# Performance work log

Measured on AMD Instinct MI355X. Metric: run time of the kernel, lower is better.

## Reference

```python
import jax, jax.numpy as jnp
import numpy as np

H = 128
N = 100000
E = 1000000
IN_DIM = 2 * H + 2


def setup_inputs() -> dict:
    key = jax.random.key(0)
    ks = jax.random.split(key, 10)
    node_embed = jax.random.normal(ks[0], (N, H), dtype=jnp.float32)
    edge_index_score = jax.random.randint(ks[1], (2, E), 0, N, dtype=jnp.int64)
    edge_attr_score = jax.random.uniform(ks[2], (E, 2), dtype=jnp.float32)
    # MLP params (kaiming-ish scale)
    W1 = jax.random.normal(ks[3], (IN_DIM, H), dtype=jnp.float32) / np.sqrt(IN_DIM)
    b1 = jnp.zeros((H,), dtype=jnp.float32)
    ln_gamma = jnp.ones((H,), dtype=jnp.float32)
    ln_beta = jnp.zeros((H,), dtype=jnp.float32)
    W2 = jax.random.normal(ks[4], (H, H // 2), dtype=jnp.float32) / np.sqrt(H)
    b2 = jnp.zeros((H // 2,), dtype=jnp.float32)
    W3 = jax.random.normal(ks[5], (H // 2, 1), dtype=jnp.float32) / np.sqrt(H // 2)
    b3 = jnp.zeros((1,), dtype=jnp.float32)
    return {
        "node_embed": node_embed,
        "edge_index_score": edge_index_score,
        "edge_attr_score": edge_attr_score,
        "W1": W1, "b1": b1, "ln_gamma": ln_gamma, "ln_beta": ln_beta,
        "W2": W2, "b2": b2, "W3": W3, "b3": b3,
    }


def _layernorm(x, gamma, beta, eps=1e-5):
    mu = jnp.mean(x, axis=-1, keepdims=True)
    var = jnp.mean(jnp.square(x - mu), axis=-1, keepdims=True)
    return (x - mu) * jax.lax.rsqrt(var + eps) * gamma + beta


def reference(node_embed, edge_index_score, edge_attr_score,
              W1, b1, ln_gamma, ln_beta, W2, b2, W3, b3):
    i_idx = edge_index_score[0]
    j_idx = edge_index_score[1]
    # [E, 2H+2]
    e_in = jnp.concatenate([node_embed[i_idx], node_embed[j_idx], edge_attr_score], axis=-1)
    h = _layernorm(e_in @ W1 + b1, ln_gamma, ln_beta)
    h = jax.nn.relu(h)  # dropout is identity in eval mode
    h = jax.nn.relu(h @ W2 + b2)
    logit = h @ W3 + b3
    return logit.squeeze(-1)  # [E]
```

## Files before the change

### kernel.cpp

```cpp
#include <hip/hip_runtime.h>
#include <hip/hip_bf16.h>
#include <hip/hip_fp16.h>

typedef __attribute__((ext_vector_type(8))) short short8;
typedef __attribute__((ext_vector_type(4))) float f32x4;
typedef _Float16 h2v __attribute__((ext_vector_type(2)));
typedef _Float16 h8v __attribute__((ext_vector_type(8)));
typedef unsigned short ushort_t;

namespace {

constexpr int H     = 128;
constexpr int E     = 1000000;
constexpr int NNODE = 100000;
constexpr int EB    = 512;
constexpr int NTILE = (E + EB - 1) / EB;
constexpr int GRID  = 256;
constexpr int TPB   = NTILE / GRID;
constexpr int REM   = NTILE - TPB * GRID;

constexpr size_t AT_OFF  = 0;
constexpr size_t AT_SZ   = (size_t)NNODE * 256 * 2;
constexpr size_t W1F_OFF = AT_SZ;
constexpr size_t W1F_SZ  = 64 * 64 * 8 * 2;
constexpr size_t W2F_OFF = W1F_OFF + W1F_SZ;
constexpr size_t W2F_SZ  = 20 * 64 * 8 * 2;
constexpr size_t WS_NEED = W2F_OFF + W2F_SZ;

__device__ __forceinline__ ushort_t f2bf(float x) {
    unsigned u = __float_as_uint(x);
    return (ushort_t)((u + 0x7FFFu + ((u >> 16) & 1u)) >> 16);
}
__device__ __forceinline__ unsigned pkbf(float a, float b) {
    __hip_bfloat162 t = __float22bfloat162_rn(make_float2(a, b));
    return *reinterpret_cast<unsigned*>(&t);
}
__device__ __forceinline__ unsigned pkhf(float a, float b) {
    __half2 t = __float22half2_rn(make_float2(a, b));
    return *reinterpret_cast<unsigned*>(&t);
}
__device__ __forceinline__ int imin(int a, int b) { return a < b ? a : b; }

union FragU { int4 i; short8 s; };
union SlotU { short8 s; h2v h[4]; };
union H8U   { h8v v; h2v h[4]; int4 i; };
union U32H  { unsigned u; h2v h; };

typedef const __attribute__((address_space(1))) unsigned int* gptr_t;
typedef __attribute__((address_space(3))) unsigned int* lptr_t;

__device__ __forceinline__ void gload16(const void* g, void* l) {
    __builtin_amdgcn_global_load_lds((gptr_t)g, (lptr_t)l, 16, 0, 0);
}

__global__ void cvt_wfrag(const float* __restrict__ W1, const float* __restrict__ W2,
                          const float* __restrict__ b2,
                          ushort_t* __restrict__ w1f, ushort_t* __restrict__ w2f) {
    int u = blockIdx.x, l = threadIdx.x;
    int lo = l & 15, hi = l >> 4;
    if (u < 64) {
        int s = u >> 3, n = u & 7, col = n * 16 + lo;
#pragma unroll
        for (int j = 0; j < 8; ++j) {
            int kk = s * 32 + hi * 8 + j;
            w1f[(u * 64 + l) * 8 + j] = f2bf(W1[kk * 128 + col]);
        }
    } else {
        int u2 = u - 64;
        int s = u2 >> 2, n = u2 & 3, col = n * 16 + lo;
#pragma unroll
        for (int j = 0; j < 8; ++j) {
            int kk = s * 32 + hi * 8 + j;
            float v = (kk < 128) ? W2[kk * 64 + col]
                    : (kk == 128 ? b2[col] : 0.f);
            __half hh = __float2half_rn(v);
            w2f[(u2 * 64 + l) * 8 + j] = *reinterpret_cast<ushort_t*>(&hh);
        }
    }
}

struct PrepSm { ushort_t w1f[32768]; };

__global__ __launch_bounds__(512, 2)
void build_atab(const float* __restrict__ ne, const ushort_t* __restrict__ w1fg,
                const float* __restrict__ b1, ushort_t* __restrict__ atab) {
    __shared__ PrepSm sm;
    const int tid = threadIdx.x;
    {
        const uint4* s1 = reinterpret_cast<const uint4*>(w1fg);
        uint4*       d1 = reinterpret_cast<uint4*>(sm.w1f);
#pragma unroll
        for (int i = 0; i < 8; ++i) d1[i * 512 + tid] = s1[i * 512 + tid];
    }
    __syncthreads();

    const int wid = tid >> 6, lane = tid & 63;
    const int lo = lane & 15, hi = lane >> 4;
    const int nbase = blockIdx.x * 512 + wid * 64;
    const f32x4 z4 = {0.f, 0.f, 0.f, 0.f};

    short8 nf[4][4];
#pragma unroll
    for (int mt = 0; mt < 4; ++mt) {
        int node = imin(nbase + mt * 16 + lo, NNODE - 1);
        const float* row = ne + (size_t)node * H;
#pragma unroll
        for (int s = 0; s < 4; ++s) {
            f32x4 a = *reinterpret_cast<const f32x4*>(row + s * 32 + hi * 8);
            f32x4 b = *reinterpret_cast<const f32x4*>(row + s * 32 + hi * 8 + 4);
            FragU f;
            f.i = make_int4((int)pkbf(a[0], a[1]), (int)pkbf(a[2], a[3]),
                            (int)pkbf(b[0], b[1]), (int)pkbf(b[2], b[3]));
            nf[mt][s] = f.s;
        }
    }

#pragma unroll
    for (int X = 0; X < 2; ++X) {
        f32x4 acc[4][8];
        if (X == 0) {
#pragma unroll
            for (int n = 0; n < 8; ++n) {
                f32x4 b1v = *reinterpret_cast<const f32x4*>(b1 + n * 16 + hi * 4);
#pragma unroll
                for (int mt = 0; mt < 4; ++mt) acc[mt][n] = b1v;
            }
        } else {
#pragma unroll
            for (int mt = 0; mt < 4; ++mt)
#pragma unroll
                for (int n = 0; n < 8; ++n) acc[mt][n] = z4;
        }
#pragma unroll
        for (int s = 0; s < 4; ++s)
#pragma unroll
            for (int n = 0; n < 8; ++n) {
                short8 wa = *reinterpret_cast<const short8*>(
                    sm.w1f + (((X * 4 + s) * 8 + n) * 64 + lane) * 8);
#pragma unroll
                for (int mt = 0; mt < 4; ++mt)
                    acc[mt][n] = __builtin_amdgcn_mfma_f32_16x16x32_bf16(wa, nf[mt][s], acc[mt][n], 0, 0, 0);
            }
#pragma unroll
        for (int mt = 0; mt < 4; ++mt) {
            int node = nbase + mt * 16 + lo;
            if (node < NNODE) {
                ushort_t* dst = atab + (size_t)node * 256 + X * 128;
#pragma unroll
                for (int n = 0; n < 8; ++n) {
                    uint2 v = make_uint2(pkhf(acc[mt][n][0], acc[mt][n][1]),
                                         pkhf(acc[mt][n][2], acc[mt][n][3]));
                    *reinterpret_cast<uint2*>(dst + n * 16 + hi * 4) = v;
                }
            }
        }
    }
}

struct __align__(16) SmemT {
    char     gbuf[8][2][8192];
    ushort_t w2f[10240];
    unsigned t0h[64], t1h[64], gh[64], bh[64];
    float    w3s[64];
};

#define GISSUE(slotp, iv, jv)                                                   \
    {                                                                           \
        const ushort_t* gi_ = atab + (size_t)(iv) * 256 + hi * 8;               \
        const ushort_t* gj_ = atab + (size_t)(jv) * 256 + 128 + hi * 8;         \
        char* lb_ = (slotp);                                                    \
        _Pragma("unroll")                                                       \
        for (int s_ = 0; s_ < 4; ++s_) gload16(gi_ + s_ * 32, lb_ + s_ * 1024); \
        _Pragma("unroll")                                                       \
        for (int s_ = 0; s_ < 4; ++s_) gload16(gj_ + s_ * 32, lb_ + 4096 + s_ * 1024); \
    }

#define SUBTILE(MT, slotp, WAITLIT, IV, JV)                                     \
    {                                                                           \
        asm volatile("s_waitcnt " WAITLIT ::: "memory");                        \
        __builtin_amdgcn_sched_barrier(0);                                      \
        const _Float16 axs = (_Float16)av[MT].x;                                \
        const _Float16 ays = (_Float16)av[MT].y;                                \
        const h2v ax2 = {axs, axs};                                             \
        const h2v ay2 = {ays, ays};                                             \
        float s1 = 0.f, s2v = 0.f;                                              \
        h2v x2[4][4];                                                           \
        _Pragma("unroll")                                                       \
        for (int s = 0; s < 4; ++s) {                                           \
            SlotU ui, uj;                                                       \
            ui.s = *reinterpret_cast<const short8*>((slotp) + s * 1024 + lane * 16);        \
            uj.s = *reinterpret_cast<const short8*>((slotp) + 4096 + s * 1024 + lane * 16); \
            uint4 t0p = *reinterpret_cast<const uint4*>(sm.t0h + s * 16 + hi * 4); \
            uint4 t1p = *reinterpret_cast<const uint4*>(sm.t1h + s * 16 + hi * 4); \
            const unsigned t0a[4] = {t0p.x, t0p.y, t0p.z, t0p.w};               \
            const unsigned t1a[4] = {t1p.x, t1p.y, t1p.z, t1p.w};               \
            _Pragma("unroll")                                                   \
            for (int p = 0; p < 4; ++p) {                                       \
                U32H w0; w0.u = t0a[p];                                         \
                U32H w1; w1.u = t1a[p];                                         \
                h2v t = ui.h[p] + uj.h[p];                                      \
                t = __builtin_elementwise_fma(ax2, w0.h, t);                    \
                t = __builtin_elementwise_fma(ay2, w1.h, t);                    \
                x2[s][p] = t;                                                   \
                s1  = __builtin_amdgcn_fdot2(t, one2, s1, false);               \
                s2v = __builtin_amdgcn_fdot2(t, t, s2v, false);                 \
            }                                                                   \
        }                                                                       \
                  \
        asm volatile("s_waitcnt lgkmcnt(0)" ::: "memory");                      \
        __builtin_amdgcn_sched_barrier(0);                                      \
        GISSUE(slotp, IV, JV);                                                  \
        __builtin_amdgcn_sched_barrier(0);                                      \
        s1 += __shfl_xor(s1, 16); s1 += __shfl_xor(s1, 32);                     \
        s2v += __shfl_xor(s2v, 16); s2v += __shfl_xor(s2v, 32);                 \
        float mean = s1 * (1.f / 128.f);                                        \
        float var  = s2v * (1.f / 128.f) - mean * mean;                         \
        float rstd = rsqrtf(var + 1e-5f);                                       \
        const _Float16 rs_ = (_Float16)rstd;                                    \
        const _Float16 cs_ = (_Float16)(-mean * rstd);                          \
        const h2v rs2 = {rs_, rs_};                                             \
        const h2v cs2 = {cs_, cs_};                                             \
        h8v hfr[4];                                                             \
        _Pragma("unroll")                                                       \
        for (int s = 0; s < 4; ++s) {                                           \
            uint4 gp = *reinterpret_cast<const uint4*>(sm.gh + s * 16 + hi * 4); \
            uint4 bp = *reinterpret_cast<const uint4*>(sm.bh + s * 16 + hi * 4); \
            const unsigned ga[4] = {gp.x, gp.y, gp.z, gp.w};                    \
            const unsigned ba[4] = {bp.x, bp.y, bp.z, bp.w};                    \
            H8U f;                                                              \
            _Pragma("unroll")                                                   \
            for (int p = 0; p < 4; ++p) {                                       \
                U32H g_; g_.u = ga[p];                                          \
                U32H b_; b_.u = ba[p];                                          \
                h2v t = __builtin_elementwise_fma(x2[s][p], rs2, cs2);          \
                t = __builtin_elementwise_fma(t, g_.h, b_.h);                   \
                t = __builtin_elementwise_max(t, zero2);                        \
                f.h[p] = t;                                                     \
            }                                                                   \
            hfr[s] = f.v;                                                       \
        }                                                                       \
        f32x4 a2[4];                                                            \
        _Pragma("unroll")                                                       \
        for (int n2 = 0; n2 < 4; ++n2) a2[n2] = zero4;                          \
        __builtin_amdgcn_s_setprio(1);                                          \
        _Pragma("unroll")                                                       \
        for (int s = 0; s < 4; ++s) {                                           \
            _Pragma("unroll")                                                   \
            for (int n2 = 0; n2 < 4; ++n2) {                                    \
                h8v wa = *reinterpret_cast<const h8v*>(sm.w2f + ((s * 4 + n2) * 64 + lane) * 8); \
                a2[n2] = __builtin_amdgcn_mfma_f32_16x16x32_f16(wa, hfr[s], a2[n2], 0, 0, 0); \
            }                                                                   \
        }                                                                       \
        {                                                                       \
            H8U cf; cf.i = make_int4(hi == 0 ? 0x00003C00 : 0, 0, 0, 0);        \
            _Pragma("unroll")                                                   \
            for (int n2 = 0; n2 < 4; ++n2) {                                    \
                h8v wa = *reinterpret_cast<const h8v*>(sm.w2f + ((16 + n2) * 64 + lane) * 8); \
                a2[n2] = __builtin_amdgcn_mfma_f32_16x16x32_f16(wa, cf.v, a2[n2], 0, 0, 0);   \
            }                                                                   \
        }                                                                       \
        __builtin_amdgcn_s_setprio(0);                                          \
        float part = 0.f;                                                       \
        _Pragma("unroll")                                                       \
        for (int n2 = 0; n2 < 4; ++n2) {                                        \
            f32x4 w3v = *reinterpret_cast<const f32x4*>(sm.w3s + n2 * 16 + hi * 4); \
            _Pragma("unroll")                                                   \
            for (int r = 0; r < 4; ++r)                                         \
                part = fmaf(fmaxf(a2[n2][r], 0.f), w3v[r], part);               \
        }                                                                       \
        part += __shfl_xor(part, 16);                                           \
        part += __shfl_xor(part, 32);                                           \
        if (hi == 0) {                                                          \
            int e = tb + (MT) * 16 + lo;                                        \
            if (e < E) out[e] = part + b3s;                                     \
        }                                                                       \
    }

__global__ __launch_bounds__(512, 2)
void edge_mlp_mfma(const ushort_t* __restrict__ atab,
                   const ushort_t* __restrict__ w2fg,
                   const int*      __restrict__ eidx,
                   const float*    __restrict__ attr,
                   const float*    __restrict__ W1,
                   const float*    __restrict__ gamma_,
                   const float*    __restrict__ beta_,
                   const float*    __restrict__ W3,
                   const float*    __restrict__ b3,
                   float*          __restrict__ out) {
    __shared__ SmemT sm;
    const int tid = threadIdx.x;
    const int bid = blockIdx.x;

    {
        const uint4* s2 = reinterpret_cast<const uint4*>(w2fg);
        uint4*       d2 = reinterpret_cast<uint4*>(sm.w2f);
        for (int i = tid; i < 1280; i += 512) d2[i] = s2[i];
    }
    if (tid < 64) {
        sm.t0h[tid] = pkhf(W1[256 * H + 2 * tid], W1[256 * H + 2 * tid + 1]);
        sm.t1h[tid] = pkhf(W1[257 * H + 2 * tid], W1[257 * H + 2 * tid + 1]);
        sm.gh[tid]  = pkhf(gamma_[2 * tid], gamma_[2 * tid + 1]);
        sm.bh[tid]  = pkhf(beta_[2 * tid], beta_[2 * tid + 1]);
        sm.w3s[tid] = W3[tid];
    }
    __syncthreads();

    const int wid = tid >> 6;
    const int lane = tid & 63;
    const int lo = lane & 15, hi = lane >> 4;
    const int ebl = wid * 64;
    const int nk = (bid < REM) ? TPB + 1 : TPB;
    char* slot0 = sm.gbuf[wid][0];
    char* slot1 = sm.gbuf[wid][1];
    const float2* attr2 = reinterpret_cast<const float2*>(attr);
    const float b3s = b3[0];
    const f32x4 zero4 = {0.f, 0.f, 0.f, 0.f};
    const h2v one2  = {(_Float16)1.f, (_Float16)1.f};
    const h2v zero2 = {(_Float16)0.f, (_Float16)0.f};

    int ci[4], cj[4], ni[4], nj[4];
    float2 av[4], avn[4];

    {
        int tb0 = bid * EB + ebl;
#pragma unroll
        for (int mt = 0; mt < 4; ++mt) {
            int e = imin(tb0 + mt * 16 + lo, E - 1);
            ci[mt] = eidx[e]; cj[mt] = eidx[E + e];
            av[mt] = attr2[e];
        }
    }
    GISSUE(slot0, ci[0], cj[0]);
    GISSUE(slot1, ci[1], cj[1]);
    {
        int tb1 = (bid + imin(1, nk - 1) * GRID) * EB + ebl;
#pragma unroll
        for (int mt = 0; mt < 4; ++mt) {
            int e = imin(tb1 + mt * 16 + lo, E - 1);
            ni[mt] = eidx[e]; nj[mt] = eidx[E + e];
            avn[mt] = attr2[e];
        }
    }

    for (int k = 0; k < nk; ++k) {
        const int tb = (bid + k * GRID) * EB + ebl;

        SUBTILE(0, slot0, "vmcnt(20)", ci[2], cj[2]);
        SUBTILE(1, slot1, "vmcnt(20)", ci[3], cj[3]);
        SUBTILE(2, slot0, "vmcnt(10)", ni[0], nj[0]);
        SUBTILE(3, slot1, "vmcnt(10)", ni[1], nj[1]);

#pragma unroll
        for (int mt = 0; mt < 4; ++mt) { ci[mt] = ni[mt]; cj[mt] = nj[mt]; av[mt] = avn[mt]; }
        {
            int t2 = imin(k + 2, nk - 1);
            int tb2 = (bid + t2 * GRID) * EB + ebl;
#pragma unroll
            for (int mt = 0; mt < 4; ++mt) {
                int e = imin(tb2 + mt * 16 + lo, E - 1);
                ni[mt] = eidx[e]; nj[mt] = eidx[E + e];
                avn[mt] = attr2[e];
            }
        }
    }
}

}

extern "C" void kernel_launch(void* const* d_in, const int* in_sizes, int n_in,
                              void* d_out, int out_size, void* d_ws, size_t ws_size,
                              hipStream_t stream) {
    const float* node_embed = (const float*)d_in[0];
    const int*   eidx       = (const int*)  d_in[1];
    const float* attr       = (const float*)d_in[2];
    const float* W1         = (const float*)d_in[3];
    const float* b1         = (const float*)d_in[4];
    const float* gamma      = (const float*)d_in[5];
    const float* beta       = (const float*)d_in[6];
    const float* W2         = (const float*)d_in[7];
    const float* b2         = (const float*)d_in[8];
    const float* W3         = (const float*)d_in[9];
    const float* b3         = (const float*)d_in[10];
    float* out = (float*)d_out;

    if (ws_size < WS_NEED) return;

    char* ws = (char*)d_ws;
    ushort_t* atab = (ushort_t*)(ws + AT_OFF);
    ushort_t* w1f  = (ushort_t*)(ws + W1F_OFF);
    ushort_t* w2f  = (ushort_t*)(ws + W2F_OFF);

    cvt_wfrag<<<84, 64, 0, stream>>>(W1, W2, b2, w1f, w2f);
    build_atab<<<(NNODE + 511) / 512, 512, 0, stream>>>(node_embed, w1f, b1, atab);
    edge_mlp_mfma<<<GRID, 512, 0, stream>>>(atab, w2f, eidx, attr, W1,
                                            gamma, beta, W3, b3, out);
}
```

Before: 117.4 us.

## Split subtile into load/reduce and normalize/MFMA phases to issue gathers earlier

Each subtile is split into a phase that reads the gathered rows from LDS and computes the layer-1 sums, and a phase that does the LayerNorm, ReLU, MFMA and output. The next gather into a slot is issued as soon as its LDS data is consumed, and the normalize/MFMA phases of earlier subtiles are deferred so they overlap with outstanding gathers. The aim is to hide global gather latency behind more independent compute. In exchange, up to four sets of intermediate activations stay live in registers, which may raise VGPR pressure or cause spills. The vmcnt wait thresholds are also retuned for the new issue order.

```diff
diff --git a/kernel.cpp b/kernel.cpp
--- a/kernel.cpp
+++ b/kernel.cpp
@@ -175,16 +175,20 @@
         for (int s_ = 0; s_ < 4; ++s_) gload16(gj_ + s_ * 32, lb_ + 4096 + s_ * 1024); \
     }
 
-#define SUBTILE(MT, slotp, WAITLIT, IV, JV)                                     \
+#define GFI(slotp, IV, JV)                                                      \
+    asm volatile("s_waitcnt lgkmcnt(0)" ::: "memory");                          \
+    __builtin_amdgcn_sched_barrier(0);                                          \
+    GISSUE(slotp, IV, JV);
+
+#define SUBA(SET, MT, slotp, WAITLIT)                                           \
+    asm volatile("s_waitcnt " WAITLIT ::: "memory");                            \
+    __builtin_amdgcn_sched_barrier(0);                                          \
     {                                                                           \
-        asm volatile("s_waitcnt " WAITLIT ::: "memory");                        \
-        __builtin_amdgcn_sched_barrier(0);                                      \
         const _Float16 axs = (_Float16)av[MT].x;                                \
         const _Float16 ays = (_Float16)av[MT].y;                                \
         const h2v ax2 = {axs, axs};                                             \
         const h2v ay2 = {ays, ays};                                             \
-        float s1 = 0.f, s2v = 0.f;                                              \
-        h2v x2[4][4];                                                           \
+        float s1t = 0.f, s2t = 0.f;                                             \
         _Pragma("unroll")                                                       \
         for (int s = 0; s < 4; ++s) {                                           \
             SlotU ui, uj;                                                       \
@@ -201,20 +205,21 @@
                 h2v t = ui.h[p] + uj.h[p];                                      \
                 t = __builtin_elementwise_fma(ax2, w0.h, t);                    \
                 t = __builtin_elementwise_fma(ay2, w1.h, t);                    \
-                x2[s][p] = t;                                                   \
-                s1  = __builtin_amdgcn_fdot2(t, one2, s1, false);               \
-                s2v = __builtin_amdgcn_fdot2(t, t, s2v, false);                 \
+                x2_##SET[s][p] = t;                                             \
+                s1t = __builtin_amdgcn_fdot2(t, one2, s1t, false);              \
+                s2t = __builtin_amdgcn_fdot2(t, t, s2t, false);                 \
             }                                                                   \
         }                                                                       \
-                  \
-        asm volatile("s_waitcnt lgkmcnt(0)" ::: "memory");                      \
-        __builtin_amdgcn_sched_barrier(0);                                      \
-        GISSUE(slotp, IV, JV);                                                  \
-        __builtin_amdgcn_sched_barrier(0);                                      \
-        s1 += __shfl_xor(s1, 16); s1 += __shfl_xor(s1, 32);                     \
-        s2v += __shfl_xor(s2v, 16); s2v += __shfl_xor(s2v, 32);                 \
-        float mean = s1 * (1.f / 128.f);                                        \
-        float var  = s2v * (1.f / 128.f) - mean * mean;                         \
+        s1_##SET = s1t; s2_##SET = s2t;                                         \
+    }
+
+#define SUBB(SET, MT)                                                           \
+    {                                                                           \
+        float a_ = s1_##SET, b_ = s2_##SET;                                     \
+        a_ += __shfl_xor(a_, 16); a_ += __shfl_xor(a_, 32);                     \
+        b_ += __shfl_xor(b_, 16); b_ += __shfl_xor(b_, 32);                     \
+        float mean = a_ * (1.f / 128.f);                                        \
+        float var  = b_ * (1.f / 128.f) - mean * mean;                          \
         float rstd = rsqrtf(var + 1e-5f);                                       \
         const _Float16 rs_ = (_Float16)rstd;                                    \
         const _Float16 cs_ = (_Float16)(-mean * rstd);                          \
@@ -231,9 +236,9 @@
             _Pragma("unroll")                                                   \
             for (int p = 0; p < 4; ++p) {                                       \
                 U32H g_; g_.u = ga[p];                                          \
-                U32H b_; b_.u = ba[p];                                          \
-                h2v t = __builtin_elementwise_fma(x2[s][p], rs2, cs2);          \
-                t = __builtin_elementwise_fma(t, g_.h, b_.h);                   \
+                U32H bb_; bb_.u = ba[p];                                        \
+                h2v t = __builtin_elementwise_fma(x2_##SET[s][p], rs2, cs2);    \
+                t = __builtin_elementwise_fma(t, g_.h, bb_.h);                  \
                 t = __builtin_elementwise_max(t, zero2);                        \
                 f.h[p] = t;                                                     \
             }                                                                   \
@@ -321,6 +326,9 @@
     int ci[4], cj[4], ni[4], nj[4];
     float2 av[4], avn[4];
 
+    h2v x2_0[4][4], x2_1[4][4], x2_2[4][4], x2_3[4][4];
+    float s1_0, s2_0, s1_1, s2_1, s1_2, s2_2, s1_3, s2_3;
+
     {
         int tb0 = bid * EB + ebl;
 #pragma unroll
@@ -345,10 +353,18 @@
     for (int k = 0; k < nk; ++k) {
         const int tb = (bid + k * GRID) * EB + ebl;
 
-        SUBTILE(0, slot0, "vmcnt(20)", ci[2], cj[2]);
-        SUBTILE(1, slot1, "vmcnt(20)", ci[3], cj[3]);
-        SUBTILE(2, slot0, "vmcnt(10)", ni[0], nj[0]);
-        SUBTILE(3, slot1, "vmcnt(10)", ni[1], nj[1]);
+        SUBA(0, 0, slot0, "vmcnt(20)");
+        GFI(slot0, ci[2], cj[2]);
+        SUBA(1, 1, slot1, "vmcnt(20)");
+        GFI(slot1, ci[3], cj[3]);
+
+        SUBA(2, 2, slot0, "vmcnt(8)");
+        SUBB(0, 0);
+        GFI(slot0, ni[0], nj[0]);
+
+        SUBA(3, 3, slot1, "vmcnt(8)");
+        SUBB(1, 1);
+        GFI(slot1, ni[1], nj[1]);
 
 #pragma unroll
         for (int mt = 0; mt < 4; ++mt) { ci[mt] = ni[mt]; cj[mt] = nj[mt]; av[mt] = avn[mt]; }
@@ -362,6 +378,9 @@
                 avn[mt] = attr2[e];
             }
         }
+
+        SUBB(2, 2);
+        SUBB(3, 3);
     }
 }
 
```

Result: slower. 122.8 us (+4.6%).
